# Optimization experiments

Measured on AMD Instinct MI355X. Metric: run time of the kernel, lower is better.

Reference implementation:

```python
import jax, jax.numpy as jnp
import numpy as np

DIST = 45
HID = 128
NLAYERS = 4
BATCH = 128


def _build_edges(d):
    n = d * d - 1
    sqrt_n = int(np.sqrt(n)) + 1
    src, dst = [], []
    for i in range(n):
        row, col = i // sqrt_n, i % sqrt_n
        for dr, dc in ((-1, 0), (1, 0), (0, -1), (0, 1)):
            nr, nc = row + dr, col + dc
            j = nr * sqrt_n + nc
            if 0 <= nr < sqrt_n and 0 <= j < n and j != i:
                src.append(i)
                dst.append(j)
    return np.asarray(src, np.int32), np.asarray(dst, np.int32), n


def setup_inputs() -> dict:
    key = jax.random.key(0)
    ks = jax.random.split(key, 8)
    src, dst, n = _build_edges(DIST)
    s = 1.0 / np.sqrt(HID)
    return {
        "x": jax.random.normal(ks[0], (BATCH, n), jnp.float32),
        "W_embed": jax.random.normal(ks[1], (1, HID), jnp.float32),
        "b_embed": jnp.zeros((HID,), jnp.float32),
        "gnn_W": jax.random.normal(ks[2], (NLAYERS, 2 * HID, HID), jnp.float32) * s,
        "gnn_b": jnp.zeros((NLAYERS, HID), jnp.float32),
        "ln_g": jnp.ones((NLAYERS, HID), jnp.float32),
        "ln_b": jnp.zeros((NLAYERS, HID), jnp.float32),
        "out_W1": jax.random.normal(ks[3], (HID, HID), jnp.float32) * s,
        "out_b1": jnp.zeros((HID,), jnp.float32),
        "out_W2": jax.random.normal(ks[4], (HID, 2), jnp.float32) * s,
        "out_b2": jnp.zeros((2,), jnp.float32),
        "edge_src": jnp.asarray(src),
        "edge_dst": jnp.asarray(dst),
    }


def _layer_norm(h, g, b, eps=1e-5):
    mu = h.mean(-1, keepdims=True)
    var = ((h - mu) ** 2).mean(-1, keepdims=True)
    return (h - mu) * jax.lax.rsqrt(var + eps) * g + b


def _segment_mean(h, src, dst, n_nodes):
    # h: [B, N, H] -> mean of incoming-neighbor features per node; 0 if no edge.
    hs = jnp.swapaxes(h[:, src, :], 0, 1)                 # [E, B, H]
    sums = jax.ops.segment_sum(hs, dst, num_segments=n_nodes)   # [N, B, H]
    cnt = jax.ops.segment_sum(jnp.ones_like(dst, jnp.float32), dst,
                              num_segments=n_nodes)              # [N]
    agg = jnp.where(cnt[:, None, None] > 0,
                    sums / jnp.maximum(cnt, 1.0)[:, None, None], 0.0)
    return jnp.swapaxes(agg, 0, 1)                        # [B, N, H]


def reference(x, W_embed, b_embed, gnn_W, gnn_b, ln_g, ln_b,
              out_W1, out_b1, out_W2, out_b2, edge_src, edge_dst):
    n_nodes = x.shape[1]
    # node_embed: Linear(1, H) applied to x[..., None]
    h = x[..., None] * W_embed[0] + b_embed               # [B, N, H]
    for l in range(gnn_W.shape[0]):
        agg = _segment_mean(h, edge_src, edge_dst, n_nodes)
        combined = jnp.concatenate([h, agg], axis=-1)     # [B, N, 2H]
        h = jax.nn.relu(combined @ gnn_W[l] + gnn_b[l])
        h = _layer_norm(h, ln_g[l], ln_b[l])
    graph_repr = h.mean(axis=1)                           # [B, H]
    hid = jax.nn.relu(graph_repr @ out_W1 + out_b1)
    return hid @ out_W2 + out_b2                          # [B, 2]
```

## Files before the change

### kernel.cpp

```cpp
#include <hip/hip_runtime.h>

typedef unsigned short u16;
typedef unsigned int   u32;
typedef __attribute__((ext_vector_type(8))) short short8;
typedef __attribute__((ext_vector_type(4))) float f32x4;

#define NN   2024
#define NB   128
#define HID  128
#define MT   128
#define MTOT (NN*NB)
#define NBLK (MTOT/MT)

__device__ __forceinline__ float bflo(u32 w){ union{u32 u; float f;}c; c.u=w<<16;        return c.f; }
__device__ __forceinline__ float bfhi(u32 w){ union{u32 u; float f;}c; c.u=w&0xffff0000u; return c.f; }
__device__ __forceinline__ float bf2f(u16 h){ union{u32 u; float f;}c; c.u=((u32)h)<<16; return c.f; }
__device__ __forceinline__ u16 f2bf(float f){ union{float f; u32 u;}c; c.f=f; return (u16)((c.u+0x7fffu+((c.u>>16)&1u))>>16); }
__device__ __forceinline__ u32 cvtpk(float lo, float hi){
  u32 r; asm("v_cvt_pk_bf16_f32 %0, %1, %2" : "=v"(r) : "v"(lo), "v"(hi)); return r;
}
__device__ __forceinline__ f32x4 mfma16(short8 a, short8 b, f32x4 c){
  return __builtin_amdgcn_mfma_f32_16x16x32_bf16(a,b,c,0,0,0);
}
__device__ __forceinline__ void glds16(const void* g, void* l){
  __builtin_amdgcn_global_load_lds((const __attribute__((address_space(1))) void*)g,
                                   (__attribute__((address_space(3))) void*)l, 16, 0, 0);
}

__device__ __forceinline__ short8 avg4(short8 a0, short8 a1, short8 a2, short8 a3,
                                       float w0, float w1, float w2, float w3){
  union{short8 s; u32 u[4];} A, B, C, D, R;
  A.s=a0; B.s=a1; C.s=a2; D.s=a3;
#pragma unroll
  for (int p=0;p<4;++p){
    float lo = w0*bflo(A.u[p]); lo = fmaf(w1,bflo(B.u[p]),lo); lo = fmaf(w2,bflo(C.u[p]),lo); lo = fmaf(w3,bflo(D.u[p]),lo);
    float hi = w0*bfhi(A.u[p]); hi = fmaf(w1,bfhi(B.u[p]),hi); hi = fmaf(w2,bfhi(C.u[p]),hi); hi = fmaf(w3,bfhi(D.u[p]),hi);
    R.u[p] = cvtpk(lo, hi);
  }
  return R.s;
}

__device__ __forceinline__ short8 synthf(float xv, float4 w0, float4 w1, float4 b0, float4 b1){
  union{short8 s; u32 u[4];} R;
  R.u[0] = cvtpk(fmaf(xv,w0.x,b0.x), fmaf(xv,w0.y,b0.y));
  R.u[1] = cvtpk(fmaf(xv,w0.z,b0.z), fmaf(xv,w0.w,b0.w));
  R.u[2] = cvtpk(fmaf(xv,w1.x,b1.x), fmaf(xv,w1.y,b1.y));
  R.u[3] = cvtpk(fmaf(xv,w1.z,b1.z), fmaf(xv,w1.w,b1.w));
  return R.s;
}

template<int EMBED>
__global__ __launch_bounds__(512, 4)
void layer3_k(const u16* __restrict__ hin, const float* __restrict__ x,
              const float* __restrict__ We, const float* __restrict__ be,
              const u16* __restrict__ Wt, const float* __restrict__ bias,
              const float* __restrict__ lng, const float* __restrict__ lnb,
              u16* __restrict__ hout)
{
  __shared__ __align__(16) char Wb[65536];
  const int t  = threadIdx.x;
  const int l  = t & 63;
  const int wv = t >> 6, wr = wv >> 1, wc = wv & 1;
  const int cB = l & 15, rg = l >> 4;

  const int orig = blockIdx.x;
  const int m0 = ((orig & 7)*253 + (orig >> 3)) * MT;

  {
    const int gl = l >> 5, gc = l & 31;
#pragma unroll
    for (int i = 0; i < 8; ++i){
      const int col = 16*wv + 2*i + gl;
      const int cs  = gc ^ (col & 7);
      glds16(Wt + (u32)col*256 + (u32)cs*8, Wb + (u32)(wv*8 + i)*1024);
    }
  }

  u32 offS[2], offN[2][4];
  float nw[2][4];
  float xs[2], mx[2];
#pragma unroll
  for (int m = 0; m < 2; ++m){
    const int row = m0 + 32*wr + 16*m + cB;
    const int nd  = row % NN;
    const int v0 = (nd >= 45), v1 = (nd <= NN-46), v2 = (nd >= 1), v3 = (nd <= NN-2);
    const int cnt = v0+v1+v2+v3;
    const float inv = (cnt==4) ? 0.25f : ((cnt==3) ? (1.f/3.f) : 0.5f);
    nw[m][0] = v0 ? inv : 0.f; nw[m][1] = v1 ? inv : 0.f;
    nw[m][2] = v2 ? inv : 0.f; nw[m][3] = v3 ? inv : 0.f;
    const int r0 = v0 ? row-45 : row, r1 = v1 ? row+45 : row;
    const int r2 = v2 ? row-1  : row, r3 = v3 ? row+1  : row;
    offS[m]    = (u32)row * 256u;
    offN[m][0] = (u32)r0 * 256u; offN[m][1] = (u32)r1 * 256u;
    offN[m][2] = (u32)r2 * 256u; offN[m][3] = (u32)r3 * 256u;
    if constexpr (EMBED){
      xs[m] = x[row];
      mx[m] = nw[m][0]*x[r0] + nw[m][1]*x[r1] + nw[m][2]*x[r2] + nw[m][3]*x[r3];
    }
  }

  f32x4 acc[2][4];
#pragma unroll
  for (int m = 0; m < 2; ++m)
#pragma unroll
    for (int j = 0; j < 4; ++j)
      acc[m][j] = (f32x4){0.f,0.f,0.f,0.f};

  __syncthreads();

  const char* hb  = (const char*)hin;
  const u32 wsz   = ((u32)(cB & 7)) << 4;
  const u32 rg16  = ((u32)rg) << 4;
  const char* wp[4];
#pragma unroll
  for (int j = 0; j < 4; ++j)
    wp[j] = Wb + (u32)(64*wc + 16*j + cB)*512;

  short8 sC0, sC1;
  if constexpr (!EMBED){
    sC0 = *(const short8*)(hb + offS[0] + rg16);
    sC1 = *(const short8*)(hb + offS[1] + rg16);
  }

#pragma unroll
  for (int ks = 0; ks < 4; ++ks){
    const u32 kb = (u32)ks*64 + rg16;
    short8 n00,n01,n02,n03, n10,n11,n12,n13;
    float4 we0, we1, bb0, bb1;
    if constexpr (!EMBED){
      n00 = *(const short8*)(hb + offN[0][0] + kb);
      n01 = *(const short8*)(hb + offN[0][1] + kb);
      n02 = *(const short8*)(hb + offN[0][2] + kb);
      n03 = *(const short8*)(hb + offN[0][3] + kb);
      n10 = *(const short8*)(hb + offN[1][0] + kb);
      n11 = *(const short8*)(hb + offN[1][1] + kb);
      n12 = *(const short8*)(hb + offN[1][2] + kb);
      n13 = *(const short8*)(hb + offN[1][3] + kb);
    } else {
      we0 = *(const float4*)(We + ks*32 + rg*8);
      we1 = *(const float4*)(We + ks*32 + rg*8 + 4);
      bb0 = *(const float4*)(be + ks*32 + rg*8);
      bb1 = *(const float4*)(be + ks*32 + rg*8 + 4);
      sC0 = synthf(xs[0], we0, we1, bb0, bb1);
      sC1 = synthf(xs[1], we0, we1, bb0, bb1);
    }
    short8 sN0, sN1;
    if constexpr (!EMBED){
      if (ks < 3){
        sN0 = *(const short8*)(hb + offS[0] + kb + 64);
        sN1 = *(const short8*)(hb + offS[1] + kb + 64);
      }
    }
    {
      const u32 a0 = kb ^ wsz;
#pragma unroll
      for (int j = 0; j < 4; ++j){
        short8 w = *(const short8*)(wp[j] + a0);
        acc[0][j] = mfma16(sC0, w, acc[0][j]);
        acc[1][j] = mfma16(sC1, w, acc[1][j]);
      }
    }
    short8 ag0, ag1;
    if constexpr (!EMBED){
      ag0 = avg4(n00,n01,n02,n03, nw[0][0],nw[0][1],nw[0][2],nw[0][3]);
      ag1 = avg4(n10,n11,n12,n13, nw[1][0],nw[1][1],nw[1][2],nw[1][3]);
    } else {
      ag0 = synthf(mx[0], we0, we1, bb0, bb1);
      ag1 = synthf(mx[1], we0, we1, bb0, bb1);
    }
    {
      const u32 a1 = (kb + 256u) ^ wsz;
#pragma unroll
      for (int j = 0; j < 4; ++j){
        short8 w = *(const short8*)(wp[j] + a1);
        acc[0][j] = mfma16(ag0, w, acc[0][j]);
        acc[1][j] = mfma16(ag1, w, acc[1][j]);
      }
    }
    if constexpr (!EMBED){
      if (ks < 3){ sC0 = sN0; sC1 = sN1; }
    }
  }

  __syncthreads();
  float2* red = (float2*)Wb;
  char* trB   = Wb + 4096;

  float b4[4], g4[4], bt4[4];
#pragma unroll
  for (int j = 0; j < 4; ++j){
    const int col = 64*wc + 16*j + cB;
    b4[j] = bias[col]; g4[j] = lng[col]; bt4[j] = lnb[col];
  }

#pragma unroll
  for (int m = 0; m < 2; ++m){
#pragma unroll
    for (int rr = 0; rr < 4; ++rr){
      float s1 = 0.f, s2 = 0.f;
#pragma unroll
      for (int j = 0; j < 4; ++j){
        float y = fmaxf(acc[m][j][rr] + b4[j], 0.f);
        acc[m][j][rr] = y;
        s1 += y; s2 += y*y;
      }
      s1 += __shfl_xor(s1,1); s1 += __shfl_xor(s1,2);
      s1 += __shfl_xor(s1,4); s1 += __shfl_xor(s1,8);
      s2 += __shfl_xor(s2,1); s2 += __shfl_xor(s2,2);
      s2 += __shfl_xor(s2,4); s2 += __shfl_xor(s2,8);
      if (cB == 0){
        const int row = 32*wr + 16*m + 4*rg + rr;
        red[row*2 + wc] = make_float2(s1, s2);
      }
    }
  }
  __syncthreads();

#pragma unroll
  for (int m = 0; m < 2; ++m){
#pragma unroll
    for (int rr = 0; rr < 4; ++rr){
      const int row = 32*wr + 16*m + 4*rg + rr;
      const float2 A = red[row*2], B = red[row*2 + 1];
      const float s1 = A.x + B.x, s2 = A.y + B.y;
      const float muv = s1 * (1.f/128.f);
      const float var = s2 * (1.f/128.f) - muv*muv;
      const float rsv = rsqrtf(var + 1e-5f);
      const u32 sw = ((u32)(row & 7)) << 4;
      char* rowp = trB + (u32)row*256;
#pragma unroll
      for (int j = 0; j < 4; ++j){
        const float y = fmaf((acc[m][j][rr]-muv)*rsv, g4[j], bt4[j]);
        const float p = __shfl_xor(y, 1);
        const u32 pk = (cB & 1) ? cvtpk(p, y) : cvtpk(y, p);
        const u32 off = ((u32)(128*wc + 32*j + 2*(cB & ~1))) ^ sw;
        *(u32*)(rowp + off) = pk;
      }
    }
  }
  __syncthreads();

  const int r = t >> 2, q = t & 3;
  const u32 sw2 = ((u32)(r & 7)) << 4;
  u16* dst = hout + (size_t)(m0 + r)*HID + q*32;
  const char* srow = trB + (u32)r*256;
#pragma unroll
  for (int i = 0; i < 4; ++i)
    *(short8*)(dst + i*8) = *(const short8*)(srow + (((u32)(q*64 + i*16)) ^ sw2));
}

__global__ void prep_k(const float* __restrict__ gw, u16* __restrict__ Wt){
  const int idx = blockIdx.x*256 + threadIdx.x;
  const int lay = idx >> 15;
  const int r   = idx & 32767;
  const int j   = r >> 8;
  const int k   = r & 255;
  Wt[idx] = f2bf(gw[lay*32768 + k*128 + j]);
}

__global__ void mean1_k(const u16* __restrict__ h, float* __restrict__ partial){
  __shared__ float red[16][16][8];
  const int blk = blockIdx.x;
  const int b = blk >> 3, s = blk & 7;
  const int t = threadIdx.x;
  const int cg = t & 15, q = t >> 4;
  const int nbeg = s*253, nend = nbeg + 253;
  float a[8] = {0.f,0.f,0.f,0.f,0.f,0.f,0.f,0.f};
  const u16* hb = h + (size_t)b * NN * HID;
  for (int n = nbeg + q; n < nend; n += 16){
    short8 v = *(const short8*)(hb + (size_t)n*HID + cg*8);
#pragma unroll
    for (int i = 0; i < 8; ++i) a[i] += bf2f((u16)v[i]);
  }
#pragma unroll
  for (int i = 0; i < 8; ++i) red[q][cg][i] = a[i];
  __syncthreads();
  if (t < 128){
    const int cc = t >> 3, i = t & 7;
    float v = 0.f;
#pragma unroll
    for (int qq = 0; qq < 16; ++qq) v += red[qq][cc][i];
    partial[((size_t)b*8 + s)*128 + t] = v;
  }
}

__global__ void mean2_k(const float* __restrict__ partial, float* __restrict__ gr){
  const int idx = blockIdx.x*256 + threadIdx.x;
  const int b = idx >> 7, c = idx & 127;
  float a = 0.f;
#pragma unroll
  for (int s = 0; s < 8; ++s) a += partial[((size_t)b*8 + s)*128 + c];
  gr[idx] = a * (1.0f / 2024.0f);
}

__global__ void head1_k(const float* __restrict__ gr, const float* __restrict__ W1,
                        const float* __restrict__ b1, float* __restrict__ hid){
  const int idx = blockIdx.x*256 + threadIdx.x;
  const int b = idx >> 7, j = idx & 127;
  const float* g = gr + b*128;
  float a = b1[j];
  for (int k = 0; k < 128; ++k) a = fmaf(g[k], W1[k*128 + j], a);
  hid[idx] = fmaxf(a, 0.f);
}

__global__ void head2_k(const float* __restrict__ hid, const float* __restrict__ W2,
                        const float* __restrict__ b2, float* __restrict__ out){
  const int t = threadIdx.x;
  const int b = t >> 1, o = t & 1;
  const float* hh = hid + b*128;
  float a = b2[o];
  for (int k = 0; k < 128; ++k) a = fmaf(hh[k], W2[k*2 + o], a);
  out[t] = a;
}

extern "C" void kernel_launch(void* const* d_in, const int* in_sizes, int n_in,
                              void* d_out, int out_size, void* d_ws, size_t ws_size,
                              hipStream_t stream){
  const float* x  = (const float*)d_in[0];
  const float* We = (const float*)d_in[1];
  const float* be = (const float*)d_in[2];
  const float* gW = (const float*)d_in[3];
  const float* gb = (const float*)d_in[4];
  const float* lg = (const float*)d_in[5];
  const float* lb = (const float*)d_in[6];
  const float* W1 = (const float*)d_in[7];
  const float* b1 = (const float*)d_in[8];
  const float* W2 = (const float*)d_in[9];
  const float* b2 = (const float*)d_in[10];
  float* out = (float*)d_out;

  char* w = (char*)d_ws;
  const size_t HB = (size_t)MTOT * HID * 2;
  u16*   hA  = (u16*)w;
  u16*   hB  = (u16*)(w + HB);
  u16*   Wt  = (u16*)(w + 2*HB);
  float* gr  = (float*)(w + 2*HB + 262144);
  float* hid = (float*)(w + 2*HB + 262144 + 65536);
  float* partial = (float*)w;

  prep_k<<<512, 256, 0, stream>>>(gW, Wt);
  layer3_k<1><<<NBLK, 512, 0, stream>>>(nullptr, x, We, be, Wt,
                                        gb, lg, lb, hA);
  layer3_k<0><<<NBLK, 512, 0, stream>>>(hA, nullptr, nullptr, nullptr, Wt + 32768,
                                        gb + 128, lg + 128, lb + 128, hB);
  layer3_k<0><<<NBLK, 512, 0, stream>>>(hB, nullptr, nullptr, nullptr, Wt + 65536,
                                        gb + 256, lg + 256, lb + 256, hA);
  layer3_k<0><<<NBLK, 512, 0, stream>>>(hA, nullptr, nullptr, nullptr, Wt + 98304,
                                        gb + 384, lg + 384, lb + 384, hB);
  mean1_k<<<NB*8, 256, 0, stream>>>(hB, partial);
  mean2_k<<<64, 256, 0, stream>>>(partial, gr);
  head1_k<<<64, 256, 0, stream>>>(gr, W1, b1, hid);
  head2_k<<<1, 256, 0, stream>>>(hid, W2, b2, out);
}
```

Measured before the change: 383.3 us.

## Collapse first layer to rank-1 form and restructure GNN layer kernel

Layer 1 is rewritten algebraically: because the embedding is linear in x, the combined matmul becomes xv*u0 + mx*u1 + c, with the vectors precomputed by a small prep kernel. A lightweight elementwise kernel then does ReLU and LayerNorm without MFMA. The remaining layers move to 256-thread blocks with 4x4 MFMA tiles per wave. Neighbour aggregates are computed once into LDS, and the weight halves are staged in two phases inside a 64KB LDS buffer. This removes redundant matmul work in layer 1 and changes how neighbour loads are reused, at the cost of lower thread count and more register pressure.

```diff
diff --git a/kernel.cpp b/kernel.cpp
--- a/kernel.cpp
+++ b/kernel.cpp
@@ -27,7 +27,7 @@
                                    (__attribute__((address_space(3))) void*)l, 16, 0, 0);
 }
 
-__device__ __forceinline__ short8 avg4(short8 a0, short8 a1, short8 a2, short8 a3,
+__device__ __forceinline__ short8 aggc(short8 a0, short8 a1, short8 a2, short8 a3,
                                        float w0, float w1, float w2, float w3){
   union{short8 s; u32 u[4];} A, B, C, D, R;
   A.s=a0; B.s=a1; C.s=a2; D.s=a3;
@@ -40,161 +40,156 @@
   return R.s;
 }
 
-__device__ __forceinline__ short8 synthf(float xv, float4 w0, float4 w1, float4 b0, float4 b1){
-  union{short8 s; u32 u[4];} R;
-  R.u[0] = cvtpk(fmaf(xv,w0.x,b0.x), fmaf(xv,w0.y,b0.y));
-  R.u[1] = cvtpk(fmaf(xv,w0.z,b0.z), fmaf(xv,w0.w,b0.w));
-  R.u[2] = cvtpk(fmaf(xv,w1.x,b1.x), fmaf(xv,w1.y,b1.y));
-  R.u[3] = cvtpk(fmaf(xv,w1.z,b1.z), fmaf(xv,w1.w,b1.w));
-  return R.s;
-}
-
-template<int EMBED>
-__global__ __launch_bounds__(512, 4)
-void layer3_k(const u16* __restrict__ hin, const float* __restrict__ x,
-              const float* __restrict__ We, const float* __restrict__ be,
-              const u16* __restrict__ Wt, const float* __restrict__ bias,
-              const float* __restrict__ lng, const float* __restrict__ lnb,
-              u16* __restrict__ hout)
+__global__ __launch_bounds__(256, 2)
+void layerG_k(const u16* __restrict__ hin, const u16* __restrict__ Wt,
+              const float* __restrict__ bias, const float* __restrict__ lng,
+              const float* __restrict__ lnb, u16* __restrict__ hout)
 {
-  __shared__ __align__(16) char Wb[65536];
+  __shared__ __align__(16) char lds[65536];
+  char* Wl = lds;
+  char* Ag = lds + 32768;
+
   const int t  = threadIdx.x;
   const int l  = t & 63;
-  const int wv = t >> 6, wr = wv >> 1, wc = wv & 1;
+  const int wv = t >> 6;
+  const int wr = wv >> 1, wc = wv & 1;
   const int cB = l & 15, rg = l >> 4;
 
   const int orig = blockIdx.x;
   const int m0 = ((orig & 7)*253 + (orig >> 3)) * MT;
 
+  const char* hb = (const char*)hin;
+
   {
-    const int gl = l >> 5, gc = l & 31;
 #pragma unroll
     for (int i = 0; i < 8; ++i){
-      const int col = 16*wv + 2*i + gl;
-      const int cs  = gc ^ (col & 7);
-      glds16(Wt + (u32)col*256 + (u32)cs*8, Wb + (u32)(wv*8 + i)*1024);
-    }
-  }
-
-  u32 offS[2], offN[2][4];
-  float nw[2][4];
-  float xs[2], mx[2];
-#pragma unroll
-  for (int m = 0; m < 2; ++m){
-    const int row = m0 + 32*wr + 16*m + cB;
-    const int nd  = row % NN;
-    const int v0 = (nd >= 45), v1 = (nd <= NN-46), v2 = (nd >= 1), v3 = (nd <= NN-2);
-    const int cnt = v0+v1+v2+v3;
-    const float inv = (cnt==4) ? 0.25f : ((cnt==3) ? (1.f/3.f) : 0.5f);
-    nw[m][0] = v0 ? inv : 0.f; nw[m][1] = v1 ? inv : 0.f;
-    nw[m][2] = v2 ? inv : 0.f; nw[m][3] = v3 ? inv : 0.f;
-    const int r0 = v0 ? row-45 : row, r1 = v1 ? row+45 : row;
-    const int r2 = v2 ? row-1  : row, r3 = v3 ? row+1  : row;
-    offS[m]    = (u32)row * 256u;
-    offN[m][0] = (u32)r0 * 256u; offN[m][1] = (u32)r1 * 256u;
-    offN[m][2] = (u32)r2 * 256u; offN[m][3] = (u32)r3 * 256u;
-    if constexpr (EMBED){
-      xs[m] = x[row];
-      mx[m] = nw[m][0]*x[r0] + nw[m][1]*x[r1] + nw[m][2]*x[r2] + nw[m][3]*x[r3];
-    }
-  }
-
-  f32x4 acc[2][4];
-#pragma unroll
-  for (int m = 0; m < 2; ++m)
+      const int slot = wv*8 + i;
+      const int col  = slot*4 + (l >> 4);
+      const u32 se   = (u32)col*256 + ((((u32)(l & 15))*8) ^ (((u32)(col & 7))<<3));
+      glds16(Wt + se, Wl + (u32)slot*1024);
+    }
+  }
+
+  const int r  = t >> 1;
+  const int hf = t & 1;
+  const int grow = m0 + r;
+  const int nd = grow % NN;
+  const int v0 = (nd >= 45), v1 = (nd <= NN-46), v2 = (nd >= 1), v3 = (nd <= NN-2);
+  const int cnt = v0+v1+v2+v3;
+  const float inv = (cnt==4) ? 0.25f : ((cnt==3) ? (1.f/3.f) : 0.5f);
+  const float w0 = v0 ? inv : 0.f, w1 = v1 ? inv : 0.f;
+  const float w2 = v2 ? inv : 0.f, w3 = v3 ? inv : 0.f;
+  const u32 nb0 = (u32)(v0 ? grow-45 : grow)*256u + (u32)hf*128u;
+  const u32 nb1 = (u32)(v1 ? grow+45 : grow)*256u + (u32)hf*128u;
+  const u32 nb2 = (u32)(v2 ? grow-1  : grow)*256u + (u32)hf*128u;
+  const u32 nb3 = (u32)(v3 ? grow+1  : grow)*256u + (u32)hf*128u;
+
+  short8 nA[4], nB_[4], nC[4], nD[4];
+#pragma unroll
+  for (int c = 0; c < 4; ++c){
+    nA[c]  = *(const short8*)(hb + nb0 + c*16);
+    nB_[c] = *(const short8*)(hb + nb1 + c*16);
+    nC[c]  = *(const short8*)(hb + nb2 + c*16);
+    nD[c]  = *(const short8*)(hb + nb3 + c*16);
+  }
+
+  f32x4 acc[4][4];
+#pragma unroll
+  for (int m = 0; m < 4; ++m)
 #pragma unroll
     for (int j = 0; j < 4; ++j)
       acc[m][j] = (f32x4){0.f,0.f,0.f,0.f};
 
   __syncthreads();
 
-  const char* hb  = (const char*)hin;
-  const u32 wsz   = ((u32)(cB & 7)) << 4;
-  const u32 rg16  = ((u32)rg) << 4;
+  const int c1 = t >> 1, hk = t & 1;
+  short8 w1r[8];
+  {
+    const u16* s1p = Wt + (u32)c1*256 + 128 + (u32)hk*64;
+#pragma unroll
+    for (int i = 0; i < 8; ++i) w1r[i] = *(const short8*)(s1p + i*8);
+  }
+
+  const u32 kswz = ((u32)(cB & 7)) << 4;
   const char* wp[4];
 #pragma unroll
   for (int j = 0; j < 4; ++j)
-    wp[j] = Wb + (u32)(64*wc + 16*j + cB)*512;
-
-  short8 sC0, sC1;
-  if constexpr (!EMBED){
-    sC0 = *(const short8*)(hb + offS[0] + rg16);
-    sC1 = *(const short8*)(hb + offS[1] + rg16);
-  }
+    wp[j] = Wl + (u32)(64*wc + 16*j + cB)*256;
+  const char* selfp = hb + ((u32)(m0 + 64*wr + cB))*256u + (u32)rg*16;
 
 #pragma unroll
   for (int ks = 0; ks < 4; ++ks){
-    const u32 kb = (u32)ks*64 + rg16;
-    short8 n00,n01,n02,n03, n10,n11,n12,n13;
-    float4 we0, we1, bb0, bb1;
-    if constexpr (!EMBED){
-      n00 = *(const short8*)(hb + offN[0][0] + kb);
-      n01 = *(const short8*)(hb + offN[0][1] + kb);
-      n02 = *(const short8*)(hb + offN[0][2] + kb);
-      n03 = *(const short8*)(hb + offN[0][3] + kb);
-      n10 = *(const short8*)(hb + offN[1][0] + kb);
-      n11 = *(const short8*)(hb + offN[1][1] + kb);
-      n12 = *(const short8*)(hb + offN[1][2] + kb);
-      n13 = *(const short8*)(hb + offN[1][3] + kb);
-    } else {
-      we0 = *(const float4*)(We + ks*32 + rg*8);
-      we1 = *(const float4*)(We + ks*32 + rg*8 + 4);
-      bb0 = *(const float4*)(be + ks*32 + rg*8);
-      bb1 = *(const float4*)(be + ks*32 + rg*8 + 4);
-      sC0 = synthf(xs[0], we0, we1, bb0, bb1);
-      sC1 = synthf(xs[1], we0, we1, bb0, bb1);
-    }
-    short8 sN0, sN1;
-    if constexpr (!EMBED){
-      if (ks < 3){
-        sN0 = *(const short8*)(hb + offS[0] + kb + 64);
-        sN1 = *(const short8*)(hb + offS[1] + kb + 64);
+    const u32 ka = ((u32)ks*64 + (u32)rg*16) ^ kswz;
+    short8 wf[4];
+#pragma unroll
+    for (int j = 0; j < 4; ++j) wf[j] = *(const short8*)(wp[j] + ka);
+#pragma unroll
+    for (int m = 0; m < 4; ++m){
+      short8 s = *(const short8*)(selfp + m*4096 + ks*64);
+#pragma unroll
+      for (int j = 0; j < 4; ++j) acc[m][j] = mfma16(s, wf[j], acc[m][j]);
+    }
+  }
+
+  {
+    char* arow = Ag + (u32)r*256;
+    const u32 asw = ((u32)(r & 7)) << 4;
+#pragma unroll
+    for (int c = 0; c < 4; ++c){
+      short8 v = aggc(nA[c], nB_[c], nC[c], nD[c], w0, w1, w2, w3);
+      *(short8*)(arow + (((u32)(hf*128 + c*16)) ^ asw)) = v;
+    }
+    short8 mA[4], mB[4], mC[4], mD[4];
+#pragma unroll
+    for (int c = 0; c < 4; ++c){
+      mA[c] = *(const short8*)(hb + nb0 + 64 + c*16);
+      mB[c] = *(const short8*)(hb + nb1 + 64 + c*16);
+      mC[c] = *(const short8*)(hb + nb2 + 64 + c*16);
+      mD[c] = *(const short8*)(hb + nb3 + 64 + c*16);
+    }
+#pragma unroll
+    for (int c = 0; c < 4; ++c){
+      short8 v = aggc(mA[c], mB[c], mC[c], mD[c], w0, w1, w2, w3);
+      *(short8*)(arow + (((u32)(hf*128 + 64 + c*16)) ^ asw)) = v;
+    }
+  }
+  __syncthreads();
+
+  {
+    char* wdst = Wl + (u32)c1*256;
+#pragma unroll
+    for (int i = 0; i < 8; ++i)
+      *(short8*)(wdst + (((u32)(hk*128 + i*16)) ^ (((u32)(c1 & 7))<<4))) = w1r[i];
+  }
+  __syncthreads();
+
+  {
+    const char* agp = Ag + (u32)(64*wr + cB)*256;
+#pragma unroll
+    for (int ks = 0; ks < 4; ++ks){
+      const u32 ka = ((u32)ks*64 + (u32)rg*16) ^ kswz;
+      short8 wf[4];
+#pragma unroll
+      for (int j = 0; j < 4; ++j) wf[j] = *(const short8*)(wp[j] + ka);
+#pragma unroll
+      for (int m = 0; m < 4; ++m){
+        short8 a = *(const short8*)(agp + m*4096 + ka);
+#pragma unroll
+        for (int j = 0; j < 4; ++j) acc[m][j] = mfma16(a, wf[j], acc[m][j]);
       }
     }
-    {
-      const u32 a0 = kb ^ wsz;
-#pragma unroll
-      for (int j = 0; j < 4; ++j){
-        short8 w = *(const short8*)(wp[j] + a0);
-        acc[0][j] = mfma16(sC0, w, acc[0][j]);
-        acc[1][j] = mfma16(sC1, w, acc[1][j]);
-      }
-    }
-    short8 ag0, ag1;
-    if constexpr (!EMBED){
-      ag0 = avg4(n00,n01,n02,n03, nw[0][0],nw[0][1],nw[0][2],nw[0][3]);
-      ag1 = avg4(n10,n11,n12,n13, nw[1][0],nw[1][1],nw[1][2],nw[1][3]);
-    } else {
-      ag0 = synthf(mx[0], we0, we1, bb0, bb1);
-      ag1 = synthf(mx[1], we0, we1, bb0, bb1);
-    }
-    {
-      const u32 a1 = (kb + 256u) ^ wsz;
-#pragma unroll
-      for (int j = 0; j < 4; ++j){
-        short8 w = *(const short8*)(wp[j] + a1);
-        acc[0][j] = mfma16(ag0, w, acc[0][j]);
-        acc[1][j] = mfma16(ag1, w, acc[1][j]);
-      }
-    }
-    if constexpr (!EMBED){
-      if (ks < 3){ sC0 = sN0; sC1 = sN1; }
-    }
-  }
-
-  __syncthreads();
-  float2* red = (float2*)Wb;
-  char* trB   = Wb + 4096;
-
+  }
+  __syncthreads();
+
+  float2* red = (float2*)Wl;
   float b4[4], g4[4], bt4[4];
 #pragma unroll
   for (int j = 0; j < 4; ++j){
     const int col = 64*wc + 16*j + cB;
     b4[j] = bias[col]; g4[j] = lng[col]; bt4[j] = lnb[col];
   }
-
-#pragma unroll
-  for (int m = 0; m < 2; ++m){
+#pragma unroll
+  for (int m = 0; m < 4; ++m){
 #pragma unroll
     for (int rr = 0; rr < 4; ++rr){
       float s1 = 0.f, s2 = 0.f;
@@ -202,32 +197,32 @@
       for (int j = 0; j < 4; ++j){
         float y = fmaxf(acc[m][j][rr] + b4[j], 0.f);
         acc[m][j][rr] = y;
-        s1 += y; s2 += y*y;
+        s1 += y; s2 = fmaf(y, y, s2);
       }
       s1 += __shfl_xor(s1,1); s1 += __shfl_xor(s1,2);
       s1 += __shfl_xor(s1,4); s1 += __shfl_xor(s1,8);
       s2 += __shfl_xor(s2,1); s2 += __shfl_xor(s2,2);
       s2 += __shfl_xor(s2,4); s2 += __shfl_xor(s2,8);
       if (cB == 0){
-        const int row = 32*wr + 16*m + 4*rg + rr;
-        red[row*2 + wc] = make_float2(s1, s2);
+        const int rl = 64*wr + 16*m + 4*rg + rr;
+        red[rl*2 + wc] = make_float2(s1, s2);
       }
     }
   }
   __syncthreads();
 
 #pragma unroll
-  for (int m = 0; m < 2; ++m){
+  for (int m = 0; m < 4; ++m){
 #pragma unroll
     for (int rr = 0; rr < 4; ++rr){
-      const int row = 32*wr + 16*m + 4*rg + rr;
-      const float2 A = red[row*2], B = red[row*2 + 1];
+      const int rl = 64*wr + 16*m + 4*rg + rr;
+      const float2 A = red[rl*2], B = red[rl*2+1];
       const float s1 = A.x + B.x, s2 = A.y + B.y;
       const float muv = s1 * (1.f/128.f);
       const float var = s2 * (1.f/128.f) - muv*muv;
       const float rsv = rsqrtf(var + 1e-5f);
-      const u32 sw = ((u32)(row & 7)) << 4;
-      char* rowp = trB + (u32)row*256;
+      const u32 sw = ((u32)(rl & 7)) << 4;
+      char* rowp = Ag + (u32)rl*256;
 #pragma unroll
       for (int j = 0; j < 4; ++j){
         const float y = fmaf((acc[m][j][rr]-muv)*rsv, g4[j], bt4[j]);
@@ -240,13 +235,80 @@
   }
   __syncthreads();
 
-  const int r = t >> 2, q = t & 3;
-  const u32 sw2 = ((u32)(r & 7)) << 4;
-  u16* dst = hout + (size_t)(m0 + r)*HID + q*32;
-  const char* srow = trB + (u32)r*256;
-#pragma unroll
-  for (int i = 0; i < 4; ++i)
-    *(short8*)(dst + i*8) = *(const short8*)(srow + (((u32)(q*64 + i*16)) ^ sw2));
+  const int r2 = t >> 1, q2 = t & 1;
+  const u32 sw2 = ((u32)(r2 & 7)) << 4;
+  u16* dst = hout + (size_t)(m0 + r2)*HID + q2*64;
+  const char* srow = Ag + (u32)r2*256;
+#pragma unroll
+  for (int i = 0; i < 8; ++i)
+    *(short8*)(dst + i*8) = *(const short8*)(srow + (((u32)(q2*128 + i*16)) ^ sw2));
+}
+
+__global__ __launch_bounds__(256, 4)
+void l1_k(const float* __restrict__ x, const float* __restrict__ uvec,
+          const float* __restrict__ lng, const float* __restrict__ lnb,
+          u16* __restrict__ hout)
+{
+  __shared__ float su[384];
+  __shared__ float sg[128], sb[128];
+  const int t = threadIdx.x;
+  const int m0 = ((blockIdx.x & 7)*253 + (blockIdx.x >> 3)) * MT;
+  for (int i = t; i < 384; i += 256) su[i] = uvec[i];
+  if (t < 128){ sg[t] = lng[t]; sb[t] = lnb[t]; }
+  __syncthreads();
+
+  const int r = t >> 1, hf = t & 1;
+  const int grow = m0 + r;
+  const int nd = grow % NN;
+  const int v0 = (nd >= 45), v1 = (nd <= NN-46), v2 = (nd >= 1), v3 = (nd <= NN-2);
+  const int cnt = v0+v1+v2+v3;
+  const float inv = (cnt==4) ? 0.25f : ((cnt==3) ? (1.f/3.f) : 0.5f);
+  const float xv = x[grow];
+  float mx = 0.f;
+  if (v0) mx += x[grow-45];
+  if (v1) mx += x[grow+45];
+  if (v2) mx += x[grow-1];
+  if (v3) mx += x[grow+1];
+  mx *= inv;
+
+  const int fb = hf*64;
+  float4 yv[16];
+  float s1 = 0.f, s2 = 0.f;
+#pragma unroll
+  for (int i = 0; i < 16; ++i){
+    const float4 a = *(const float4*)(su + fb + i*4);
+    const float4 b = *(const float4*)(su + 128 + fb + i*4);
+    const float4 c = *(const float4*)(su + 256 + fb + i*4);
+    float4 y;
+    y.x = fmaxf(fmaf(xv, a.x, fmaf(mx, b.x, c.x)), 0.f);
+    y.y = fmaxf(fmaf(xv, a.y, fmaf(mx, b.y, c.y)), 0.f);
+    y.z = fmaxf(fmaf(xv, a.z, fmaf(mx, b.z, c.z)), 0.f);
+    y.w = fmaxf(fmaf(xv, a.w, fmaf(mx, b.w, c.w)), 0.f);
+    yv[i] = y;
+    s1 += y.x + y.y + y.z + y.w;
+    s2 = fmaf(y.x,y.x, fmaf(y.y,y.y, fmaf(y.z,y.z, fmaf(y.w,y.w, s2))));
+  }
+  s1 += __shfl_xor(s1, 1);
+  s2 += __shfl_xor(s2, 1);
+  const float muv = s1 * (1.f/128.f);
+  const float var = s2 * (1.f/128.f) - muv*muv;
+  const float rsv = rsqrtf(var + 1e-5f);
+
+  u16* dst = hout + (size_t)grow*HID + fb;
+#pragma unroll
+  for (int i = 0; i < 8; ++i){
+    const float4 ya = yv[2*i], yb = yv[2*i+1];
+    const float4 ga = *(const float4*)(sg + fb + i*8);
+    const float4 gb2 = *(const float4*)(sg + fb + i*8 + 4);
+    const float4 ba = *(const float4*)(sb + fb + i*8);
+    const float4 bb = *(const float4*)(sb + fb + i*8 + 4);
+    u32 o0 = cvtpk(fmaf((ya.x-muv)*rsv, ga.x, ba.x), fmaf((ya.y-muv)*rsv, ga.y, ba.y));
+    u32 o1 = cvtpk(fmaf((ya.z-muv)*rsv, ga.z, ba.z), fmaf((ya.w-muv)*rsv, ga.w, ba.w));
+    u32 o2 = cvtpk(fmaf((yb.x-muv)*rsv, gb2.x, bb.x), fmaf((yb.y-muv)*rsv, gb2.y, bb.y));
+    u32 o3 = cvtpk(fmaf((yb.z-muv)*rsv, gb2.z, bb.z), fmaf((yb.w-muv)*rsv, gb2.w, bb.w));
+    uint4 pk = make_uint4(o0, o1, o2, o3);
+    *(uint4*)(dst + i*8) = pk;
+  }
 }
 
 __global__ void prep_k(const float* __restrict__ gw, u16* __restrict__ Wt){
@@ -256,6 +318,21 @@
   const int j   = r >> 8;
   const int k   = r & 255;
   Wt[idx] = f2bf(gw[lay*32768 + k*128 + j]);
+}
+
+__global__ void prep2_k(const float* __restrict__ We, const float* __restrict__ be,
+                        const float* __restrict__ gW, const float* __restrict__ gb,
+                        float* __restrict__ uvec){
+  const int f = threadIdx.x;
+  float u0 = 0.f, u1 = 0.f, c = 0.f;
+  for (int k = 0; k < 128; ++k){
+    const float a = gW[k*128 + f];
+    const float b = gW[(128+k)*128 + f];
+    u0 = fmaf(We[k], a, u0);
+    u1 = fmaf(We[k], b, u1);
+    c  = fmaf(be[k], a + b, c);
+  }
+  uvec[f] = u0; uvec[128+f] = u1; uvec[256+f] = c + gb[f];
 }
 
 __global__ void mean1_k(const u16* __restrict__ h, float* __restrict__ partial){
@@ -331,22 +408,20 @@
 
   char* w = (char*)d_ws;
   const size_t HB = (size_t)MTOT * HID * 2;
-  u16*   hA  = (u16*)w;
-  u16*   hB  = (u16*)(w + HB);
-  u16*   Wt  = (u16*)(w + 2*HB);
-  float* gr  = (float*)(w + 2*HB + 262144);
-  float* hid = (float*)(w + 2*HB + 262144 + 65536);
+  u16*   hA   = (u16*)w;
+  u16*   hB   = (u16*)(w + HB);
+  u16*   Wt   = (u16*)(w + 2*HB);
+  float* gr   = (float*)(w + 2*HB + 262144);
+  float* hid  = (float*)(w + 2*HB + 262144 + 65536);
+  float* uvec = (float*)(w + 2*HB + 262144 + 131072);
   float* partial = (float*)w;
 
+  prep2_k<<<1, 128, 0, stream>>>(We, be, gW, gb, uvec);
   prep_k<<<512, 256, 0, stream>>>(gW, Wt);
-  layer3_k<1><<<NBLK, 512, 0, stream>>>(nullptr, x, We, be, Wt,
-                                        gb, lg, lb, hA);
-  layer3_k<0><<<NBLK, 512, 0, stream>>>(hA, nullptr, nullptr, nullptr, Wt + 32768,
-                                        gb + 128, lg + 128, lb + 128, hB);
-  layer3_k<0><<<NBLK, 512, 0, stream>>>(hB, nullptr, nullptr, nullptr, Wt + 65536,
-                                        gb + 256, lg + 256, lb + 256, hA);
-  layer3_k<0><<<NBLK, 512, 0, stream>>>(hA, nullptr, nullptr, nullptr, Wt + 98304,
-                                        gb + 384, lg + 384, lb + 384, hB);
+  l1_k<<<NBLK, 256, 0, stream>>>(x, uvec, lg, lb, hA);
+  layerG_k<<<NBLK, 256, 0, stream>>>(hA, Wt + 32768, gb + 128, lg + 128, lb + 128, hB);
+  layerG_k<<<NBLK, 256, 0, stream>>>(hB, Wt + 65536, gb + 256, lg + 256, lb + 256, hA);
+  layerG_k<<<NBLK, 256, 0, stream>>>(hA, Wt + 98304, gb + 384, lg + 384, lb + 384, hB);
   mean1_k<<<NB*8, 256, 0, stream>>>(hB, partial);
   mean2_k<<<64, 256, 0, stream>>>(partial, gr);
   head1_k<<<64, 256, 0, stream>>>(gr, W1, b1, hid);
```

After: 381.8 us. About the same (-0.4%).
